# Kernel optimization log

Hardware: AMD Instinct MI355X
Metric: run time of the kernel (lower is better)

Reference implementation:

```python
import jax, jax.numpy as jnp
import numpy as np

D_MODEL = 1024
D_FF = 4096
EPS = 1e-5


def layer_norm(x, gamma, beta):
    mu = jnp.mean(x, axis=-1, keepdims=True)
    var = jnp.var(x, axis=-1, keepdims=True)
    return (x - mu) * jax.lax.rsqrt(var + EPS) * gamma + beta


def attention(x_q, x_kv, WQ, WK, WV, causal):
    Q = x_q @ WQ          # [B,Sq,D]
    K = x_kv @ WK         # [B,Sk,D]
    V = x_kv @ WV
    scale = 1.0 / jnp.sqrt(jnp.asarray(Q.shape[-1], Q.dtype))
    scores = jnp.einsum('bqd,bkd->bqk', Q, K) * scale
    if causal:
        Sq, Sk = scores.shape[-2], scores.shape[-1]
        mask = jnp.triu(jnp.full((Sq, Sk), -jnp.inf, scores.dtype), k=1)
        scores = scores + mask
    attn = jax.nn.softmax(scores, axis=-1)
    return jnp.einsum('bqk,bkd->bqd', attn, V)


def setup_inputs() -> dict:
    key = jax.random.key(0)
    ks = jax.random.split(key, 16)
    B, S = 4, 2048
    s = 0.02
    inp = {
        'y': jax.random.normal(ks[0], (B, S, D_MODEL), jnp.float32),
        'Z': jax.random.normal(ks[1], (B, S, D_MODEL), jnp.float32),
        'WQ1': jax.random.normal(ks[2], (D_MODEL, D_MODEL), jnp.float32) * s,
        'WK1': jax.random.normal(ks[3], (D_MODEL, D_MODEL), jnp.float32) * s,
        'WV1': jax.random.normal(ks[4], (D_MODEL, D_MODEL), jnp.float32) * s,
        'WQ2': jax.random.normal(ks[5], (D_MODEL, D_MODEL), jnp.float32) * s,
        'WK2': jax.random.normal(ks[6], (D_MODEL, D_MODEL), jnp.float32) * s,
        'WV2': jax.random.normal(ks[7], (D_MODEL, D_MODEL), jnp.float32) * s,
        'W_ff1': jax.random.normal(ks[8], (D_MODEL, D_FF), jnp.float32) * s,
        'b_ff1': jnp.zeros((D_FF,), jnp.float32),
        'W_ff2': jax.random.normal(ks[9], (D_FF, D_MODEL), jnp.float32) * s,
        'b_ff2': jnp.zeros((D_MODEL,), jnp.float32),
        'g1': jnp.ones((D_MODEL,), jnp.float32), 'be1': jnp.zeros((D_MODEL,), jnp.float32),
        'g2': jnp.ones((D_MODEL,), jnp.float32), 'be2': jnp.zeros((D_MODEL,), jnp.float32),
        'g3': jnp.ones((D_MODEL,), jnp.float32), 'be3': jnp.zeros((D_MODEL,), jnp.float32),
    }
    return inp


def reference(y, Z, WQ1, WK1, WV1, WQ2, WK2, WV2, W_ff1, b_ff1, W_ff2, b_ff2,
              g1, be1, g2, be2, g3, be3):
    # masked self-attention + add&norm
    y = layer_norm(y + attention(y, y, WQ1, WK1, WV1, causal=True), g1, be1)
    # cross-attention + add&norm
    y = layer_norm(y + attention(y, Z, WQ2, WK2, WV2, causal=False), g2, be2)
    # FFN + add&norm
    h = jax.nn.relu(y @ W_ff1 + b_ff1) @ W_ff2 + b_ff2
    y = layer_norm(y + h, g3, be3)
    return y
```

## Files before the change

kernel.cpp:

```cpp
#include <hip/hip_runtime.h>
#include <cstddef>

typedef unsigned short u16;
typedef __attribute__((ext_vector_type(8))) short bf16x8;
typedef __attribute__((ext_vector_type(4))) float f32x4;

__device__ __forceinline__ u16 f2bf(float f) {
  union { float f; unsigned u; } x; x.f = f;
  unsigned r = x.u + 0x7fffu + ((x.u >> 16) & 1u);
  return (u16)(r >> 16);
}
__device__ __forceinline__ float bf2f(u16 h) {
  union { unsigned u; float f; } x; x.u = ((unsigned)h) << 16;
  return x.f;
}

__device__ __forceinline__ void gll16(const u16* g, u16* ldsbase) {
  __builtin_amdgcn_global_load_lds(
      (const __attribute__((address_space(1))) void*)g,
      (__attribute__((address_space(3))) void*)ldsbase, 16, 0, 0);
}

__global__ __launch_bounds__(256) void f32_to_bf16(const float* __restrict__ in,
                                                   u16* __restrict__ out, size_t n) {
  size_t i = (size_t)blockIdx.x * 256 + threadIdx.x;
  if (i < n) out[i] = f2bf(in[i]);
}

__global__ __launch_bounds__(256) void transpose_f32_bf16(const float* __restrict__ in,
                                                          u16* __restrict__ out,
                                                          int R, int C) {
  __shared__ float tile[32][33];
  int c0 = blockIdx.x * 32, r0 = blockIdx.y * 32;
  int tx = threadIdx.x & 31, ty = threadIdx.x >> 5;
  #pragma unroll
  for (int i = ty; i < 32; i += 8)
    tile[i][tx] = in[(size_t)(r0 + i) * C + c0 + tx];
  __syncthreads();
  #pragma unroll
  for (int i = ty; i < 32; i += 8)
    out[(size_t)(c0 + i) * R + r0 + tx] = f2bf(tile[tx][i]);
}

enum { EPI_F32 = 0, EPI_BF16 = 1, EPI_BF16_SCALE = 2,
       EPI_BIAS_RELU_BF16 = 3, EPI_BIAS_F32 = 4 };
enum { MODE_FULL = 0, MODE_TRI = 1, MODE_CAUSAL_K = 2 };

template <int EPI, int MODE>
__global__ __launch_bounds__(512) void gemm256(
    const u16* __restrict__ A, const u16* __restrict__ Bt,
    void* __restrict__ C0, const float* __restrict__ bias,
    int K, int lda, int ldb, int ldc,
    long long sA, long long sB, long long sC)
{
  __shared__ __align__(16) u16 lA[2][256 * 64];
  __shared__ __align__(16) u16 lB[2][256 * 64];

  const unsigned gx = gridDim.x, gxy = gridDim.x * gridDim.y;
  unsigned id = blockIdx.x + gx * blockIdx.y + gxy * blockIdx.z;
  const unsigned nb = gxy * gridDim.z;
  unsigned p = id;
  if ((nb & 7u) == 0u) p = (id & 7u) * (nb >> 3) + (id >> 3);
  int z, mi, ni;
  if constexpr (MODE == MODE_TRI) {
    z = (int)(p / gxy);
    int r = (int)(p % gxy);
    int m = 0;
    while ((m + 1) * (m + 2) / 2 <= r) m++;
    mi = m; ni = r - m * (m + 1) / 2;
  } else {
    z = (int)(p / gxy);
    const unsigned rem = p % gxy;
    mi = (int)(rem / gx);
    ni = (int)(rem % gx);
  }
  const int m0 = mi * 256, n0 = ni * 256;

  A  += (long long)z * sA;
  Bt += (long long)z * sB;

  int NT = K >> 6;
  if constexpr (MODE == MODE_CAUSAL_K) NT = (m0 + 256) >> 6;

  const int t    = threadIdx.x;
  const int lane = t & 63;
  const int wave = t >> 6;
  const int wr   = wave >> 2;
  const int wc   = wave & 3;
  const int quad = lane >> 4;
  const int lrow = lane & 15;

  const int srow = lane >> 3;
  const int scol = ((lane & 7) ^ srow) * 8;
  const u16* gAp = A  + (size_t)(m0 + wave * 8 + srow) * lda + scol;
  const u16* gBp = Bt + (size_t)(n0 + wave * 8 + srow) * ldb + scol;
  const size_t a64 = (size_t)64 * lda, b64 = (size_t)64 * ldb;
  const int lw = wave * 512;

  const int pg0 = (quad ^ (lrow & 7)) * 8;
  const int pg1 = pg0 ^ 32;
  const int rA = (wr * 128 + lrow) * 64;
  const int rB = (wc * 64 + lrow) * 64;

  f32x4 acc[8][4];
  const f32x4 zero = {0.f, 0.f, 0.f, 0.f};
  #pragma unroll
  for (int i = 0; i < 8; i++)
    #pragma unroll
    for (int j = 0; j < 4; j++) acc[i][j] = zero;

  auto stage = [&](int b, int s, int kt) {
    const int k = kt * 64;
    if (s == 0) {
      gll16(gBp + k,            &lB[b][lw]);
      gll16(gBp + k + b64,      &lB[b][4096 + lw]);
    } else if (s == 1) {
      gll16(gBp + k + 2 * b64,  &lB[b][8192 + lw]);
      gll16(gBp + k + 3 * b64,  &lB[b][12288 + lw]);
    } else if (s == 2) {
      gll16(gAp + k,            &lA[b][lw]);
      gll16(gAp + k + a64,      &lA[b][4096 + lw]);
    } else {
      gll16(gAp + k + 2 * a64,  &lA[b][8192 + lw]);
      gll16(gAp + k + 3 * a64,  &lA[b][12288 + lw]);
    }
  };

  stage(0, 0, 0); stage(0, 1, 0); stage(0, 2, 0); stage(0, 3, 0);
  if (NT > 1) {
    stage(1, 0, 1); stage(1, 1, 1); stage(1, 2, 1);
    asm volatile("s_waitcnt vmcnt(6)" ::: "memory");
  } else {
    asm volatile("s_waitcnt vmcnt(0)" ::: "memory");
  }
  __builtin_amdgcn_s_barrier();

  bf16x8 af[4][2], bfr[4][2];

  for (int kt = 0; kt < NT; ++kt) {
    const int bsel = kt & 1;
    const u16* sa = &lA[bsel][0];
    const u16* sb = &lB[bsel][0];

    #pragma unroll
    for (int mf = 0; mf < 4; ++mf) {
      af[mf][0] = *(const bf16x8*)(sa + rA + mf * 1024 + pg0);
      af[mf][1] = *(const bf16x8*)(sa + rA + mf * 1024 + pg1);
    }
    if (wc < 2) {
      #pragma unroll
      for (int nf = 0; nf < 4; ++nf) {
        bfr[nf][0] = *(const bf16x8*)(sb + rB + nf * 1024 + pg0);
        bfr[nf][1] = *(const bf16x8*)(sb + rB + nf * 1024 + pg1);
      }
    } else {
      #pragma unroll
      for (int nf = 0; nf < 2; ++nf) {
        bfr[nf][0] = *(const bf16x8*)(sb + rB + nf * 1024 + pg0);
        bfr[nf][1] = *(const bf16x8*)(sb + rB + nf * 1024 + pg1);
      }
    }
    if (kt + 1 < NT) stage(bsel ^ 1, 3, kt + 1);
    __builtin_amdgcn_s_barrier();
    asm volatile("s_waitcnt lgkmcnt(0)" ::: "memory");
    __builtin_amdgcn_sched_barrier(0);
    __builtin_amdgcn_s_setprio(1);
    #pragma unroll
    for (int mf = 0; mf < 4; ++mf)
      #pragma unroll
      for (int nf = 0; nf < 2; ++nf) {
        acc[mf][nf] = __builtin_amdgcn_mfma_f32_16x16x32_bf16(bfr[nf][0], af[mf][0], acc[mf][nf], 0, 0, 0);
        acc[mf][nf] = __builtin_amdgcn_mfma_f32_16x16x32_bf16(bfr[nf][1], af[mf][1], acc[mf][nf], 0, 0, 0);
      }
    __builtin_amdgcn_s_setprio(0);
    __builtin_amdgcn_s_barrier();

    if (wc >= 2) {
      #pragma unroll
      for (int nf = 2; nf < 4; ++nf) {
        bfr[nf][0] = *(const bf16x8*)(sb + rB + nf * 1024 + pg0);
        bfr[nf][1] = *(const bf16x8*)(sb + rB + nf * 1024 + pg1);
      }
    }
    if (kt + 2 < NT) stage(bsel, 0, kt + 2);
    __builtin_amdgcn_s_barrier();
    asm volatile("s_waitcnt lgkmcnt(0)" ::: "memory");
    __builtin_amdgcn_sched_barrier(0);
    __builtin_amdgcn_s_setprio(1);
    #pragma unroll
    for (int mf = 0; mf < 4; ++mf)
      #pragma unroll
      for (int nf = 2; nf < 4; ++nf) {
        acc[mf][nf] = __builtin_amdgcn_mfma_f32_16x16x32_bf16(bfr[nf][0], af[mf][0], acc[mf][nf], 0, 0, 0);
        acc[mf][nf] = __builtin_amdgcn_mfma_f32_16x16x32_bf16(bfr[nf][1], af[mf][1], acc[mf][nf], 0, 0, 0);
      }
    __builtin_amdgcn_s_setprio(0);
    __builtin_amdgcn_s_barrier();

    #pragma unroll
    for (int mf = 0; mf < 4; ++mf) {
      af[mf][0] = *(const bf16x8*)(sa + rA + (mf + 4) * 1024 + pg0);
      af[mf][1] = *(const bf16x8*)(sa + rA + (mf + 4) * 1024 + pg1);
    }
    if (kt + 2 < NT) stage(bsel, 1, kt + 2);
    __builtin_amdgcn_s_barrier();
    asm volatile("s_waitcnt lgkmcnt(0)" ::: "memory");
    __builtin_amdgcn_sched_barrier(0);
    __builtin_amdgcn_s_setprio(1);
    #pragma unroll
    for (int mf = 0; mf < 4; ++mf)
      #pragma unroll
      for (int nf = 2; nf < 4; ++nf) {
        acc[mf + 4][nf] = __builtin_amdgcn_mfma_f32_16x16x32_bf16(bfr[nf][0], af[mf][0], acc[mf + 4][nf], 0, 0, 0);
        acc[mf + 4][nf] = __builtin_amdgcn_mfma_f32_16x16x32_bf16(bfr[nf][1], af[mf][1], acc[mf + 4][nf], 0, 0, 0);
      }
    __builtin_amdgcn_s_setprio(0);
    __builtin_amdgcn_s_barrier();

    if (kt + 2 < NT) {
      stage(bsel, 2, kt + 2);
      asm volatile("s_waitcnt vmcnt(6)" ::: "memory");
    } else if (kt + 1 < NT) {
      asm volatile("s_waitcnt vmcnt(0)" ::: "memory");
    }
    __builtin_amdgcn_s_barrier();
    __builtin_amdgcn_s_setprio(1);
    #pragma unroll
    for (int mf = 0; mf < 4; ++mf)
      #pragma unroll
      for (int nf = 0; nf < 2; ++nf) {
        acc[mf + 4][nf] = __builtin_amdgcn_mfma_f32_16x16x32_bf16(bfr[nf][0], af[mf][0], acc[mf + 4][nf], 0, 0, 0);
        acc[mf + 4][nf] = __builtin_amdgcn_mfma_f32_16x16x32_bf16(bfr[nf][1], af[mf][1], acc[mf + 4][nf], 0, 0, 0);
      }
    __builtin_amdgcn_s_setprio(0);
    __builtin_amdgcn_s_barrier();
  }

  const size_t zoff = (size_t)((long long)z * sC);
  #pragma unroll
  for (int mf = 0; mf < 8; ++mf) {
    #pragma unroll
    for (int nf = 0; nf < 4; ++nf) {
      const size_t m  = (size_t)(m0 + wr * 128 + mf * 16 + lrow);
      const size_t nc = (size_t)(n0 + wc * 64 + nf * 16 + quad * 4);
      const size_t idx = zoff + m * (size_t)ldc + nc;
      f32x4 v = acc[mf][nf];
      if constexpr (EPI == EPI_F32) {
        *(float4*)((float*)C0 + idx) = make_float4(v[0], v[1], v[2], v[3]);
      } else if constexpr (EPI == EPI_BF16) {
        ushort4 o; o.x = f2bf(v[0]); o.y = f2bf(v[1]); o.z = f2bf(v[2]); o.w = f2bf(v[3]);
        *(ushort4*)((u16*)C0 + idx) = o;
      } else if constexpr (EPI == EPI_BF16_SCALE) {
        ushort4 o;
        o.x = f2bf(v[0] * 0.03125f); o.y = f2bf(v[1] * 0.03125f);
        o.z = f2bf(v[2] * 0.03125f); o.w = f2bf(v[3] * 0.03125f);
        *(ushort4*)((u16*)C0 + idx) = o;
      } else if constexpr (EPI == EPI_BIAS_RELU_BF16) {
        const float4 bb = *(const float4*)(bias + nc);
        float y0 = v[0] + bb.x, y1 = v[1] + bb.y, y2 = v[2] + bb.z, y3 = v[3] + bb.w;
        ushort4 o;
        o.x = f2bf(y0 > 0.f ? y0 : 0.f); o.y = f2bf(y1 > 0.f ? y1 : 0.f);
        o.z = f2bf(y2 > 0.f ? y2 : 0.f); o.w = f2bf(y3 > 0.f ? y3 : 0.f);
        *(ushort4*)((u16*)C0 + idx) = o;
      } else {
        const float4 bb = *(const float4*)(bias + nc);
        *(float4*)((float*)C0 + idx) =
            make_float4(v[0] + bb.x, v[1] + bb.y, v[2] + bb.z, v[3] + bb.w);
      }
    }
  }
}

__global__ __launch_bounds__(256) void softmax_bf16(u16* __restrict__ SP, int causal) {
  __shared__ float red[8];
  const int row = blockIdx.x;
  const int q = row & 2047;
  u16* p = SP + (size_t)row * 2048;
  const int t = threadIdx.x;
  const int base = t * 8;
  const int limit = causal ? (q + 1) : 2048;

  uint4 raw = *(const uint4*)(p + base);
  unsigned w[4] = {raw.x, raw.y, raw.z, raw.w};
  float v[8];
  #pragma unroll
  for (int j = 0; j < 4; j++) {
    union { unsigned u; float f; } lo, hi;
    lo.u = w[j] << 16; hi.u = w[j] & 0xffff0000u;
    v[2 * j] = lo.f; v[2 * j + 1] = hi.f;
  }
  #pragma unroll
  for (int j = 0; j < 8; j++) if (base + j >= limit) v[j] = -3.4e38f;

  float mx = v[0];
  #pragma unroll
  for (int j = 1; j < 8; j++) mx = fmaxf(mx, v[j]);
  #pragma unroll
  for (int o = 32; o > 0; o >>= 1) mx = fmaxf(mx, __shfl_down(mx, o));
  if ((t & 63) == 0) red[t >> 6] = mx;
  __syncthreads();
  mx = fmaxf(fmaxf(red[0], red[1]), fmaxf(red[2], red[3]));

  float s = 0.f;
  #pragma unroll
  for (int j = 0; j < 8; j++) { float e = __expf(v[j] - mx); v[j] = e; s += e; }
  #pragma unroll
  for (int o = 32; o > 0; o >>= 1) s += __shfl_down(s, o);
  if ((t & 63) == 0) red[4 + (t >> 6)] = s;
  __syncthreads();
  const float inv = 1.f / (red[4] + red[5] + red[6] + red[7]);

  unsigned o4[4];
  #pragma unroll
  for (int j = 0; j < 4; j++)
    o4[j] = (unsigned)f2bf(v[2 * j] * inv) | ((unsigned)f2bf(v[2 * j + 1] * inv) << 16);
  *(uint4*)(p + base) = make_uint4(o4[0], o4[1], o4[2], o4[3]);
}

template <int ABF>
__global__ __launch_bounds__(256) void ln_residual(const void* __restrict__ a_,
                                                   const float* __restrict__ b,
                                                   const float* __restrict__ g,
                                                   const float* __restrict__ be,
                                                   float* __restrict__ outf,
                                                   u16* __restrict__ outb) {
  __shared__ float red[8];
  const size_t base = (size_t)blockIdx.x * 1024;
  const int t = threadIdx.x;
  const int i0 = t * 4;

  float va[4];
  if constexpr (ABF) {
    const ushort4 h = *(const ushort4*)((const u16*)a_ + base + i0);
    va[0] = bf2f(h.x); va[1] = bf2f(h.y); va[2] = bf2f(h.z); va[3] = bf2f(h.w);
  } else {
    const float4 f = *(const float4*)((const float*)a_ + base + i0);
    va[0] = f.x; va[1] = f.y; va[2] = f.z; va[3] = f.w;
  }
  const float4 vb = *(const float4*)(b + base + i0);
  float v[4] = {va[0] + vb.x, va[1] + vb.y, va[2] + vb.z, va[3] + vb.w};

  float s = v[0] + v[1] + v[2] + v[3];
  #pragma unroll
  for (int o = 32; o > 0; o >>= 1) s += __shfl_down(s, o);
  if ((t & 63) == 0) red[t >> 6] = s;
  __syncthreads();
  const float mean = (red[0] + red[1] + red[2] + red[3]) * (1.f / 1024.f);

  float qq = 0.f;
  #pragma unroll
  for (int i = 0; i < 4; i++) { float d = v[i] - mean; qq += d * d; }
  #pragma unroll
  for (int o = 32; o > 0; o >>= 1) qq += __shfl_down(qq, o);
  if ((t & 63) == 0) red[4 + (t >> 6)] = qq;
  __syncthreads();
  const float rstd = rsqrtf((red[4] + red[5] + red[6] + red[7]) * (1.f / 1024.f) + 1e-5f);

  const float4 gg = *(const float4*)(g + i0);
  const float4 bb = *(const float4*)(be + i0);
  float y0 = (v[0] - mean) * rstd * gg.x + bb.x;
  float y1 = (v[1] - mean) * rstd * gg.y + bb.y;
  float y2 = (v[2] - mean) * rstd * gg.z + bb.z;
  float y3 = (v[3] - mean) * rstd * gg.w + bb.w;
  if (outf) *(float4*)(outf + base + i0) = make_float4(y0, y1, y2, y3);
  if (outb) {
    ushort4 o4; o4.x = f2bf(y0); o4.y = f2bf(y1); o4.z = f2bf(y2); o4.w = f2bf(y3);
    *(ushort4*)(outb + base + i0) = o4;
  }
}

extern "C" void kernel_launch(void* const* d_in, const int* in_sizes, int n_in,
                              void* d_out, int out_size, void* d_ws, size_t ws_size,
                              hipStream_t stream)
{
  const float* y_in = (const float*)d_in[0];
  const float* Z_in = (const float*)d_in[1];
  const float* WQ1  = (const float*)d_in[2];
  const float* WK1  = (const float*)d_in[3];
  const float* WV1  = (const float*)d_in[4];
  const float* WQ2  = (const float*)d_in[5];
  const float* WK2  = (const float*)d_in[6];
  const float* WV2  = (const float*)d_in[7];
  const float* Wff1 = (const float*)d_in[8];
  const float* bff1 = (const float*)d_in[9];
  const float* Wff2 = (const float*)d_in[10];
  const float* bff2 = (const float*)d_in[11];
  const float* g1  = (const float*)d_in[12];
  const float* be1 = (const float*)d_in[13];
  const float* g2  = (const float*)d_in[14];
  const float* be2 = (const float*)d_in[15];
  const float* g3  = (const float*)d_in[16];
  const float* be3 = (const float*)d_in[17];
  (void)in_sizes; (void)n_in; (void)out_size;

  constexpr int Bn = 4, S = 2048, D = 1024, DF = 4096;
  constexpr long long BS = (long long)Bn * S;
  const long long SD = (long long)S * D;
  const long long SS = (long long)S * S;
  const long long SD2 = (long long)S * 2 * D;

  char* ws = (char*)d_ws;
  size_t off = 0;
  auto alloc = [&](size_t bytes) -> char* {
    char* p = ws + off;
    off += (bytes + 255) & ~(size_t)255;
    return p;
  };

  u16* wq1t  = (u16*)alloc((size_t)D * D * 2);
  u16* wk1t  = (u16*)alloc((size_t)D * D * 2);
  u16* wv1t  = (u16*)alloc((size_t)D * D * 2);
  u16* wq2t  = (u16*)alloc((size_t)D * D * 2);
  u16* wk2t  = (u16*)alloc((size_t)D * D * 2);
  u16* wv2t  = (u16*)alloc((size_t)D * D * 2);
  u16* wff1t = (u16*)alloc((size_t)D * DF * 2);
  u16* wff2t = (u16*)alloc((size_t)D * DF * 2);
  u16* ybf   = (u16*)alloc((size_t)BS * D * 2);
  u16* zbf   = (u16*)alloc((size_t)BS * D * 2);
  u16* QKb   = (u16*)alloc((size_t)BS * 2 * D * 2);
  u16* Vtb   = (u16*)alloc((size_t)D * BS * 2);
  u16* SPb   = (u16*)alloc((size_t)Bn * S * S * 2);
  float* attnF = (float*)alloc((size_t)BS * D * 4);
  u16*   y1b = ybf;
  u16*   y2b = zbf;
  u16*   Hb  = QKb;
  float* Fb  = attnF;

  if (off > ws_size) return;

  const dim3 blk(256);
  const dim3 blk512(512);

  f32_to_bf16<<<dim3((unsigned)((BS * D) / 256)), blk, 0, stream>>>(y_in, ybf, (size_t)BS * D);
  f32_to_bf16<<<dim3((unsigned)((BS * D) / 256)), blk, 0, stream>>>(Z_in, zbf, (size_t)BS * D);
  transpose_f32_bf16<<<dim3(D / 32, D / 32), blk, 0, stream>>>(WQ1, wq1t, D, D);
  transpose_f32_bf16<<<dim3(D / 32, D / 32), blk, 0, stream>>>(WK1, wk1t, D, D);
  transpose_f32_bf16<<<dim3(D / 32, D / 32), blk, 0, stream>>>(WV1, wv1t, D, D);
  transpose_f32_bf16<<<dim3(D / 32, D / 32), blk, 0, stream>>>(WQ2, wq2t, D, D);
  transpose_f32_bf16<<<dim3(D / 32, D / 32), blk, 0, stream>>>(WK2, wk2t, D, D);
  transpose_f32_bf16<<<dim3(D / 32, D / 32), blk, 0, stream>>>(WV2, wv2t, D, D);
  transpose_f32_bf16<<<dim3(DF / 32, D / 32), blk, 0, stream>>>(Wff1, wff1t, D, DF);
  transpose_f32_bf16<<<dim3(D / 32, DF / 32), blk, 0, stream>>>(Wff2, wff2t, DF, D);

  gemm256<EPI_BF16, MODE_FULL><<<dim3(2 * D / 256, BS / 256, 1), blk512, 0, stream>>>(
      ybf, wq1t, QKb, nullptr, D, D, D, 2 * D, 0, 0, 0);
  gemm256<EPI_BF16, MODE_FULL><<<dim3((unsigned)(BS / 256), D / 256, 1), blk512, 0, stream>>>(
      wv1t, ybf, Vtb, nullptr, D, D, D, (int)BS, 0, 0, 0);
  gemm256<EPI_BF16_SCALE, MODE_TRI><<<dim3(36, 1, Bn), blk512, 0, stream>>>(
      QKb, QKb + D, SPb, nullptr, D, 2 * D, 2 * D, S, SD2, SD2, SS);
  softmax_bf16<<<dim3((unsigned)(Bn * S)), blk, 0, stream>>>(SPb, 1);
  gemm256<EPI_F32, MODE_CAUSAL_K><<<dim3(D / 256, S / 256, Bn), blk512, 0, stream>>>(
      SPb, Vtb, attnF, nullptr, S, S, (int)BS, D, SS, S, SD);
  ln_residual<0><<<dim3((unsigned)BS), blk, 0, stream>>>(y_in, attnF, g1, be1, nullptr, y1b);

  gemm256<EPI_BF16, MODE_FULL><<<dim3(D / 256, BS / 256, 1), blk512, 0, stream>>>(
      y1b, wq2t, QKb, nullptr, D, D, D, 2 * D, 0, 0, 0);
  gemm256<EPI_BF16, MODE_FULL><<<dim3(D / 256, BS / 256, 1), blk512, 0, stream>>>(
      zbf, wk2t, QKb + D, nullptr, D, D, D, 2 * D, 0, 0, 0);
  gemm256<EPI_BF16, MODE_FULL><<<dim3((unsigned)(BS / 256), D / 256, 1), blk512, 0, stream>>>(
      wv2t, zbf, Vtb, nullptr, D, D, D, (int)BS, 0, 0, 0);
  gemm256<EPI_BF16_SCALE, MODE_FULL><<<dim3(S / 256, S / 256, Bn), blk512, 0, stream>>>(
      QKb, QKb + D, SPb, nullptr, D, 2 * D, 2 * D, S, SD2, SD2, SS);
  softmax_bf16<<<dim3((unsigned)(Bn * S)), blk, 0, stream>>>(SPb, 0);
  gemm256<EPI_F32, MODE_FULL><<<dim3(D / 256, S / 256, Bn), blk512, 0, stream>>>(
      SPb, Vtb, attnF, nullptr, S, S, (int)BS, D, SS, S, SD);
  ln_residual<1><<<dim3((unsigned)BS), blk, 0, stream>>>(y1b, attnF, g2, be2, nullptr, y2b);

  gemm256<EPI_BIAS_RELU_BF16, MODE_FULL><<<dim3(DF / 256, BS / 256, 1), blk512, 0, stream>>>(
      y2b, wff1t, Hb, bff1, D, D, D, DF, 0, 0, 0);
  gemm256<EPI_BIAS_F32, MODE_FULL><<<dim3(D / 256, BS / 256, 1), blk512, 0, stream>>>(
      Hb, wff2t, Fb, bff2, DF, DF, DF, D, 0, 0, 0);
  ln_residual<1><<<dim3((unsigned)BS), blk, 0, stream>>>(y2b, Fb, g3, be3, (float*)d_out, nullptr);
}
```

Measured before the change: 870.7 us.

## Template GEMM tile shape and use 256x128 tiles for low-occupancy GEMMs

```diff
diff --git a/kernel.cpp b/kernel.cpp
--- a/kernel.cpp
+++ b/kernel.cpp
@@ -46,15 +46,22 @@
        EPI_BIAS_RELU_BF16 = 3, EPI_BIAS_F32 = 4 };
 enum { MODE_FULL = 0, MODE_TRI = 1, MODE_CAUSAL_K = 2 };
 
-template <int EPI, int MODE>
+template <int EPI, int MODE, int BM, int BN>
 __global__ __launch_bounds__(512) void gemm256(
     const u16* __restrict__ A, const u16* __restrict__ Bt,
     void* __restrict__ C0, const float* __restrict__ bias,
     int K, int lda, int ldb, int ldc,
     long long sA, long long sB, long long sC)
 {
-  __shared__ __align__(16) u16 lA[2][256 * 64];
-  __shared__ __align__(16) u16 lB[2][256 * 64];
+  constexpr int WM  = BM / 128;
+  constexpr int WN  = 8 / WM;
+  constexpr int CPW = BN / WN;
+  constexpr int NF  = CPW / 16;
+  constexpr int nBr = BN / 64;
+  constexpr int nAr = BM / 64;
+
+  __shared__ __align__(16) u16 lA[2][BM * 64];
+  __shared__ __align__(16) u16 lB[2][BN * 64];
 
   const unsigned gx = gridDim.x, gxy = gridDim.x * gridDim.y;
   unsigned id = blockIdx.x + gx * blockIdx.y + gxy * blockIdx.z;
@@ -66,27 +73,32 @@
     z = (int)(p / gxy);
     int r = (int)(p % gxy);
     int m = 0;
-    while ((m + 1) * (m + 2) / 2 <= r) m++;
-    mi = m; ni = r - m * (m + 1) / 2;
+    if constexpr (BN == 256) {
+      while ((m + 1) * (m + 2) / 2 <= r) m++;
+      mi = m; ni = r - m * (m + 1) / 2;
+    } else {
+      while ((m + 1) * (m + 2) <= r) m++;
+      mi = m; ni = r - m * (m + 1);
+    }
   } else {
     z = (int)(p / gxy);
     const unsigned rem = p % gxy;
     mi = (int)(rem / gx);
     ni = (int)(rem % gx);
   }
-  const int m0 = mi * 256, n0 = ni * 256;
+  const int m0 = mi * BM, n0 = ni * BN;
 
   A  += (long long)z * sA;
   Bt += (long long)z * sB;
 
   int NT = K >> 6;
-  if constexpr (MODE == MODE_CAUSAL_K) NT = (m0 + 256) >> 6;
+  if constexpr (MODE == MODE_CAUSAL_K) NT = (m0 + BM) >> 6;
 
   const int t    = threadIdx.x;
   const int lane = t & 63;
   const int wave = t >> 6;
-  const int wr   = wave >> 2;
-  const int wc   = wave & 3;
+  const int wr   = (WM == 1) ? 0 : (wave >> 2);
+  const int wc   = (WM == 1) ? wave : (wave & 3);
   const int quad = lane >> 4;
   const int lrow = lane & 15;
 
@@ -100,149 +112,227 @@
   const int pg0 = (quad ^ (lrow & 7)) * 8;
   const int pg1 = pg0 ^ 32;
   const int rA = (wr * 128 + lrow) * 64;
-  const int rB = (wc * 64 + lrow) * 64;
-
-  f32x4 acc[8][4];
+  const int rB = (wc * CPW + lrow) * 64;
+
+  f32x4 acc[8][NF];
   const f32x4 zero = {0.f, 0.f, 0.f, 0.f};
   #pragma unroll
   for (int i = 0; i < 8; i++)
     #pragma unroll
-    for (int j = 0; j < 4; j++) acc[i][j] = zero;
-
-  auto stage = [&](int b, int s, int kt) {
-    const int k = kt * 64;
-    if (s == 0) {
-      gll16(gBp + k,            &lB[b][lw]);
-      gll16(gBp + k + b64,      &lB[b][4096 + lw]);
-    } else if (s == 1) {
-      gll16(gBp + k + 2 * b64,  &lB[b][8192 + lw]);
-      gll16(gBp + k + 3 * b64,  &lB[b][12288 + lw]);
-    } else if (s == 2) {
-      gll16(gAp + k,            &lA[b][lw]);
-      gll16(gAp + k + a64,      &lA[b][4096 + lw]);
+    for (int j = 0; j < NF; j++) acc[i][j] = zero;
+
+  bf16x8 af[4][2];
+  bf16x8 bfr[NF][2];
+
+  if constexpr (BM == 256 && BN == 256) {
+    auto stage = [&](int b, int s, int kt) {
+      const int k = kt * 64;
+      if (s == 0) {
+        gll16(gBp + k,            &lB[b][lw]);
+        gll16(gBp + k + b64,      &lB[b][4096 + lw]);
+      } else if (s == 1) {
+        gll16(gBp + k + 2 * b64,  &lB[b][8192 + lw]);
+        gll16(gBp + k + 3 * b64,  &lB[b][12288 + lw]);
+      } else if (s == 2) {
+        gll16(gAp + k,            &lA[b][lw]);
+        gll16(gAp + k + a64,      &lA[b][4096 + lw]);
+      } else {
+        gll16(gAp + k + 2 * a64,  &lA[b][8192 + lw]);
+        gll16(gAp + k + 3 * a64,  &lA[b][12288 + lw]);
+      }
+    };
+
+    stage(0, 0, 0); stage(0, 1, 0); stage(0, 2, 0); stage(0, 3, 0);
+    if (NT > 1) {
+      stage(1, 0, 1); stage(1, 1, 1); stage(1, 2, 1);
+      asm volatile("s_waitcnt vmcnt(6)" ::: "memory");
     } else {
-      gll16(gAp + k + 2 * a64,  &lA[b][8192 + lw]);
-      gll16(gAp + k + 3 * a64,  &lA[b][12288 + lw]);
-    }
-  };
-
-  stage(0, 0, 0); stage(0, 1, 0); stage(0, 2, 0); stage(0, 3, 0);
-  if (NT > 1) {
-    stage(1, 0, 1); stage(1, 1, 1); stage(1, 2, 1);
-    asm volatile("s_waitcnt vmcnt(6)" ::: "memory");
+      asm volatile("s_waitcnt vmcnt(0)" ::: "memory");
+    }
+    __builtin_amdgcn_s_barrier();
+
+    for (int kt = 0; kt < NT; ++kt) {
+      const int bsel = kt & 1;
+      const u16* sa = &lA[bsel][0];
+      const u16* sb = &lB[bsel][0];
+
+      #pragma unroll
+      for (int mf = 0; mf < 4; ++mf) {
+        af[mf][0] = *(const bf16x8*)(sa + rA + mf * 1024 + pg0);
+        af[mf][1] = *(const bf16x8*)(sa + rA + mf * 1024 + pg1);
+      }
+      if (wc < 2) {
+        #pragma unroll
+        for (int nf = 0; nf < 4; ++nf) {
+          bfr[nf][0] = *(const bf16x8*)(sb + rB + nf * 1024 + pg0);
+          bfr[nf][1] = *(const bf16x8*)(sb + rB + nf * 1024 + pg1);
+        }
+      } else {
+        #pragma unroll
+        for (int nf = 0; nf < 2; ++nf) {
+          bfr[nf][0] = *(const bf16x8*)(sb + rB + nf * 1024 + pg0);
+          bfr[nf][1] = *(const bf16x8*)(sb + rB + nf * 1024 + pg1);
+        }
+      }
+      if (kt + 1 < NT) stage(bsel ^ 1, 3, kt + 1);
+      __builtin_amdgcn_s_barrier();
+      asm volatile("s_waitcnt lgkmcnt(0)" ::: "memory");
+      __builtin_amdgcn_sched_barrier(0);
+      __builtin_amdgcn_s_setprio(1);
+      #pragma unroll
+      for (int mf = 0; mf < 4; ++mf)
+        #pragma unroll
+        for (int nf = 0; nf < 2; ++nf) {
+          acc[mf][nf] = __builtin_amdgcn_mfma_f32_16x16x32_bf16(bfr[nf][0], af[mf][0], acc[mf][nf], 0, 0, 0);
+          acc[mf][nf] = __builtin_amdgcn_mfma_f32_16x16x32_bf16(bfr[nf][1], af[mf][1], acc[mf][nf], 0, 0, 0);
+        }
+      __builtin_amdgcn_s_setprio(0);
+      __builtin_amdgcn_s_barrier();
+
+      if (wc >= 2) {
+        #pragma unroll
+        for (int nf = 2; nf < 4; ++nf) {
+          bfr[nf][0] = *(const bf16x8*)(sb + rB + nf * 1024 + pg0);
+          bfr[nf][1] = *(const bf16x8*)(sb + rB + nf * 1024 + pg1);
+        }
+      }
+      if (kt + 2 < NT) stage(bsel, 0, kt + 2);
+      __builtin_amdgcn_s_barrier();
+      asm volatile("s_waitcnt lgkmcnt(0)" ::: "memory");
+      __builtin_amdgcn_sched_barrier(0);
+      __builtin_amdgcn_s_setprio(1);
+      #pragma unroll
+      for (int mf = 0; mf < 4; ++mf)
+        #pragma unroll
+        for (int nf = 2; nf < 4; ++nf) {
+          acc[mf][nf] = __builtin_amdgcn_mfma_f32_16x16x32_bf16(bfr[nf][0], af[mf][0], acc[mf][nf], 0, 0, 0);
+          acc[mf][nf] = __builtin_amdgcn_mfma_f32_16x16x32_bf16(bfr[nf][1], af[mf][1], acc[mf][nf], 0, 0, 0);
+        }
+      __builtin_amdgcn_s_setprio(0);
+      __builtin_amdgcn_s_barrier();
+
+      #pragma unroll
+      for (int mf = 0; mf < 4; ++mf) {
+        af[mf][0] = *(const bf16x8*)(sa + rA + (mf + 4) * 1024 + pg0);
+        af[mf][1] = *(const bf16x8*)(sa + rA + (mf + 4) * 1024 + pg1);
+      }
+      if (kt + 2 < NT) stage(bsel, 1, kt + 2);
+      __builtin_amdgcn_s_barrier();
+      asm volatile("s_waitcnt lgkmcnt(0)" ::: "memory");
+      __builtin_amdgcn_sched_barrier(0);
+      __builtin_amdgcn_s_setprio(1);
+      #pragma unroll
+      for (int mf = 0; mf < 4; ++mf)
+        #pragma unroll
+        for (int nf = 2; nf < 4; ++nf) {
+          acc[mf + 4][nf] = __builtin_amdgcn_mfma_f32_16x16x32_bf16(bfr[nf][0], af[mf][0], acc[mf + 4][nf], 0, 0, 0);
+          acc[mf + 4][nf] = __builtin_amdgcn_mfma_f32_16x16x32_bf16(bfr[nf][1], af[mf][1], acc[mf + 4][nf], 0, 0, 0);
+        }
+      __builtin_amdgcn_s_setprio(0);
+      __builtin_amdgcn_s_barrier();
+
+      if (kt + 2 < NT) {
+        stage(bsel, 2, kt + 2);
+        asm volatile("s_waitcnt vmcnt(6)" ::: "memory");
+      } else if (kt + 1 < NT) {
+        asm volatile("s_waitcnt vmcnt(0)" ::: "memory");
+      }
+      __builtin_amdgcn_s_barrier();
+      __builtin_amdgcn_s_setprio(1);
+      #pragma unroll
+      for (int mf = 0; mf < 4; ++mf)
+        #pragma unroll
+        for (int nf = 0; nf < 2; ++nf) {
+          acc[mf + 4][nf] = __builtin_amdgcn_mfma_f32_16x16x32_bf16(bfr[nf][0], af[mf][0], acc[mf + 4][nf], 0, 0, 0);
+          acc[mf + 4][nf] = __builtin_amdgcn_mfma_f32_16x16x32_bf16(bfr[nf][1], af[mf][1], acc[mf + 4][nf], 0, 0, 0);
+        }
+      __builtin_amdgcn_s_setprio(0);
+      __builtin_amdgcn_s_barrier();
+    }
   } else {
-    asm volatile("s_waitcnt vmcnt(0)" ::: "memory");
-  }
-  __builtin_amdgcn_s_barrier();
-
-  bf16x8 af[4][2], bfr[4][2];
-
-  for (int kt = 0; kt < NT; ++kt) {
-    const int bsel = kt & 1;
-    const u16* sa = &lA[bsel][0];
-    const u16* sb = &lB[bsel][0];
-
-    #pragma unroll
-    for (int mf = 0; mf < 4; ++mf) {
-      af[mf][0] = *(const bf16x8*)(sa + rA + mf * 1024 + pg0);
-      af[mf][1] = *(const bf16x8*)(sa + rA + mf * 1024 + pg1);
-    }
-    if (wc < 2) {
-      #pragma unroll
-      for (int nf = 0; nf < 4; ++nf) {
-        bfr[nf][0] = *(const bf16x8*)(sb + rB + nf * 1024 + pg0);
-        bfr[nf][1] = *(const bf16x8*)(sb + rB + nf * 1024 + pg1);
-      }
+    auto stage3 = [&](int b, int h, int kt) {
+      const int k = kt * 64;
+      #pragma unroll
+      for (int s = 0; s < 3; ++s) {
+        const int rg = h * 3 + s;
+        if (rg < nBr) gll16(gBp + k + (size_t)rg * b64, &lB[b][rg * 4096 + lw]);
+        else          gll16(gAp + k + (size_t)(rg - nBr) * a64, &lA[b][(rg - nBr) * 4096 + lw]);
+      }
+    };
+
+    stage3(0, 0, 0); stage3(0, 1, 0);
+    if (NT > 1) {
+      stage3(1, 0, 1);
+      asm volatile("s_waitcnt vmcnt(3)" ::: "memory");
     } else {
+      asm volatile("s_waitcnt vmcnt(0)" ::: "memory");
+    }
+    __builtin_amdgcn_s_barrier();
+
+    for (int kt = 0; kt < NT; ++kt) {
+      const int bsel = kt & 1;
+      const u16* sa = &lA[bsel][0];
+      const u16* sb = &lB[bsel][0];
+
+      #pragma unroll
+      for (int mf = 0; mf < 4; ++mf) {
+        af[mf][0] = *(const bf16x8*)(sa + rA + mf * 1024 + pg0);
+        af[mf][1] = *(const bf16x8*)(sa + rA + mf * 1024 + pg1);
+      }
       #pragma unroll
       for (int nf = 0; nf < 2; ++nf) {
         bfr[nf][0] = *(const bf16x8*)(sb + rB + nf * 1024 + pg0);
         bfr[nf][1] = *(const bf16x8*)(sb + rB + nf * 1024 + pg1);
       }
-    }
-    if (kt + 1 < NT) stage(bsel ^ 1, 3, kt + 1);
-    __builtin_amdgcn_s_barrier();
-    asm volatile("s_waitcnt lgkmcnt(0)" ::: "memory");
-    __builtin_amdgcn_sched_barrier(0);
-    __builtin_amdgcn_s_setprio(1);
-    #pragma unroll
-    for (int mf = 0; mf < 4; ++mf)
-      #pragma unroll
-      for (int nf = 0; nf < 2; ++nf) {
-        acc[mf][nf] = __builtin_amdgcn_mfma_f32_16x16x32_bf16(bfr[nf][0], af[mf][0], acc[mf][nf], 0, 0, 0);
-        acc[mf][nf] = __builtin_amdgcn_mfma_f32_16x16x32_bf16(bfr[nf][1], af[mf][1], acc[mf][nf], 0, 0, 0);
-      }
-    __builtin_amdgcn_s_setprio(0);
-    __builtin_amdgcn_s_barrier();
-
-    if (wc >= 2) {
-      #pragma unroll
-      for (int nf = 2; nf < 4; ++nf) {
-        bfr[nf][0] = *(const bf16x8*)(sb + rB + nf * 1024 + pg0);
-        bfr[nf][1] = *(const bf16x8*)(sb + rB + nf * 1024 + pg1);
-      }
-    }
-    if (kt + 2 < NT) stage(bsel, 0, kt + 2);
-    __builtin_amdgcn_s_barrier();
-    asm volatile("s_waitcnt lgkmcnt(0)" ::: "memory");
-    __builtin_amdgcn_sched_barrier(0);
-    __builtin_amdgcn_s_setprio(1);
-    #pragma unroll
-    for (int mf = 0; mf < 4; ++mf)
-      #pragma unroll
-      for (int nf = 2; nf < 4; ++nf) {
-        acc[mf][nf] = __builtin_amdgcn_mfma_f32_16x16x32_bf16(bfr[nf][0], af[mf][0], acc[mf][nf], 0, 0, 0);
-        acc[mf][nf] = __builtin_amdgcn_mfma_f32_16x16x32_bf16(bfr[nf][1], af[mf][1], acc[mf][nf], 0, 0, 0);
-      }
-    __builtin_amdgcn_s_setprio(0);
-    __builtin_amdgcn_s_barrier();
-
-    #pragma unroll
-    for (int mf = 0; mf < 4; ++mf) {
-      af[mf][0] = *(const bf16x8*)(sa + rA + (mf + 4) * 1024 + pg0);
-      af[mf][1] = *(const bf16x8*)(sa + rA + (mf + 4) * 1024 + pg1);
-    }
-    if (kt + 2 < NT) stage(bsel, 1, kt + 2);
-    __builtin_amdgcn_s_barrier();
-    asm volatile("s_waitcnt lgkmcnt(0)" ::: "memory");
-    __builtin_amdgcn_sched_barrier(0);
-    __builtin_amdgcn_s_setprio(1);
-    #pragma unroll
-    for (int mf = 0; mf < 4; ++mf)
-      #pragma unroll
-      for (int nf = 2; nf < 4; ++nf) {
-        acc[mf + 4][nf] = __builtin_amdgcn_mfma_f32_16x16x32_bf16(bfr[nf][0], af[mf][0], acc[mf + 4][nf], 0, 0, 0);
-        acc[mf + 4][nf] = __builtin_amdgcn_mfma_f32_16x16x32_bf16(bfr[nf][1], af[mf][1], acc[mf + 4][nf], 0, 0, 0);
-      }
-    __builtin_amdgcn_s_setprio(0);
-    __builtin_amdgcn_s_barrier();
-
-    if (kt + 2 < NT) {
-      stage(bsel, 2, kt + 2);
-      asm volatile("s_waitcnt vmcnt(6)" ::: "memory");
-    } else if (kt + 1 < NT) {
-      asm volatile("s_waitcnt vmcnt(0)" ::: "memory");
-    }
-    __builtin_amdgcn_s_barrier();
-    __builtin_amdgcn_s_setprio(1);
-    #pragma unroll
-    for (int mf = 0; mf < 4; ++mf)
-      #pragma unroll
-      for (int nf = 0; nf < 2; ++nf) {
-        acc[mf + 4][nf] = __builtin_amdgcn_mfma_f32_16x16x32_bf16(bfr[nf][0], af[mf][0], acc[mf + 4][nf], 0, 0, 0);
-        acc[mf + 4][nf] = __builtin_amdgcn_mfma_f32_16x16x32_bf16(bfr[nf][1], af[mf][1], acc[mf + 4][nf], 0, 0, 0);
-      }
-    __builtin_amdgcn_s_setprio(0);
-    __builtin_amdgcn_s_barrier();
+      if (kt + 1 < NT) stage3(bsel ^ 1, 1, kt + 1);
+      __builtin_amdgcn_s_barrier();
+      asm volatile("s_waitcnt lgkmcnt(0)" ::: "memory");
+      __builtin_amdgcn_sched_barrier(0);
+      __builtin_amdgcn_s_setprio(1);
+      #pragma unroll
+      for (int mf = 0; mf < 4; ++mf)
+        #pragma unroll
+        for (int nf = 0; nf < 2; ++nf) {
+          acc[mf][nf] = __builtin_amdgcn_mfma_f32_16x16x32_bf16(bfr[nf][0], af[mf][0], acc[mf][nf], 0, 0, 0);
+          acc[mf][nf] = __builtin_amdgcn_mfma_f32_16x16x32_bf16(bfr[nf][1], af[mf][1], acc[mf][nf], 0, 0, 0);
+        }
+      __builtin_amdgcn_s_setprio(0);
+      __builtin_amdgcn_s_barrier();
+
+      #pragma unroll
+      for (int mf = 0; mf < 4; ++mf) {
+        af[mf][0] = *(const bf16x8*)(sa + rA + (mf + 4) * 1024 + pg0);
+        af[mf][1] = *(const bf16x8*)(sa + rA + (mf + 4) * 1024 + pg1);
+      }
+      if (kt + 2 < NT) {
+        stage3(bsel, 0, kt + 2);
+        asm volatile("s_waitcnt vmcnt(3)" ::: "memory");
+      } else if (kt + 1 < NT) {
+        asm volatile("s_waitcnt vmcnt(0)" ::: "memory");
+      }
+      __builtin_amdgcn_s_barrier();
+      asm volatile("s_waitcnt lgkmcnt(0)" ::: "memory");
+      __builtin_amdgcn_sched_barrier(0);
+      __builtin_amdgcn_s_setprio(1);
+      #pragma unroll
+      for (int mf = 0; mf < 4; ++mf)
+        #pragma unroll
+        for (int nf = 0; nf < 2; ++nf) {
+          acc[mf + 4][nf] = __builtin_amdgcn_mfma_f32_16x16x32_bf16(bfr[nf][0], af[mf][0], acc[mf + 4][nf], 0, 0, 0);
+          acc[mf + 4][nf] = __builtin_amdgcn_mfma_f32_16x16x32_bf16(bfr[nf][1], af[mf][1], acc[mf + 4][nf], 0, 0, 0);
+        }
+      __builtin_amdgcn_s_setprio(0);
+      __builtin_amdgcn_s_barrier();
+    }
   }
 
   const size_t zoff = (size_t)((long long)z * sC);
   #pragma unroll
   for (int mf = 0; mf < 8; ++mf) {
     #pragma unroll
-    for (int nf = 0; nf < 4; ++nf) {
+    for (int nf = 0; nf < NF; ++nf) {
       const size_t m  = (size_t)(m0 + wr * 128 + mf * 16 + lrow);
-      const size_t nc = (size_t)(n0 + wc * 64 + nf * 16 + quad * 4);
+      const size_t nc = (size_t)(n0 + wc * CPW + nf * 16 + quad * 4);
       const size_t idx = zoff + m * (size_t)ldc + nc;
       f32x4 v = acc[mf][nf];
       if constexpr (EPI == EPI_F32) {
@@ -278,19 +368,25 @@
   u16* p = SP + (size_t)row * 2048;
   const int t = threadIdx.x;
   const int base = t * 8;
-  const int limit = causal ? (q + 1) : 2048;
-
-  uint4 raw = *(const uint4*)(p + base);
-  unsigned w[4] = {raw.x, raw.y, raw.z, raw.w};
+  const int limit  = causal ? (q + 1) : 2048;
+  const int wlimit = causal ? (((q >> 8) + 1) << 8) : 2048;
+
   float v[8];
-  #pragma unroll
-  for (int j = 0; j < 4; j++) {
-    union { unsigned u; float f; } lo, hi;
-    lo.u = w[j] << 16; hi.u = w[j] & 0xffff0000u;
-    v[2 * j] = lo.f; v[2 * j + 1] = hi.f;
-  }
-  #pragma unroll
-  for (int j = 0; j < 8; j++) if (base + j >= limit) v[j] = -3.4e38f;
+  if (base < limit) {
+    uint4 raw = *(const uint4*)(p + base);
+    unsigned w[4] = {raw.x, raw.y, raw.z, raw.w};
+    #pragma unroll
+    for (int j = 0; j < 4; j++) {
+      union { unsigned u; float f; } lo, hi;
+      lo.u = w[j] << 16; hi.u = w[j] & 0xffff0000u;
+      v[2 * j] = lo.f; v[2 * j + 1] = hi.f;
+    }
+    #pragma unroll
+    for (int j = 0; j < 8; j++) if (base + j >= limit) v[j] = -3.4e38f;
+  } else {
+    #pragma unroll
+    for (int j = 0; j < 8; j++) v[j] = -3.4e38f;
+  }
 
   float mx = v[0];
   #pragma unroll
@@ -310,11 +406,13 @@
   __syncthreads();
   const float inv = 1.f / (red[4] + red[5] + red[6] + red[7]);
 
-  unsigned o4[4];
-  #pragma unroll
-  for (int j = 0; j < 4; j++)
-    o4[j] = (unsigned)f2bf(v[2 * j] * inv) | ((unsigned)f2bf(v[2 * j + 1] * inv) << 16);
-  *(uint4*)(p + base) = make_uint4(o4[0], o4[1], o4[2], o4[3]);
+  if (base < wlimit) {
+    unsigned o4[4];
+    #pragma unroll
+    for (int j = 0; j < 4; j++)
+      o4[j] = (unsigned)f2bf(v[2 * j] * inv) | ((unsigned)f2bf(v[2 * j + 1] * inv) << 16);
+    *(uint4*)(p + base) = make_uint4(o4[0], o4[1], o4[2], o4[3]);
+  }
 }
 
 template <int ABF>
@@ -442,33 +540,33 @@
   transpose_f32_bf16<<<dim3(DF / 32, D / 32), blk, 0, stream>>>(Wff1, wff1t, D, DF);
   transpose_f32_bf16<<<dim3(D / 32, DF / 32), blk, 0, stream>>>(Wff2, wff2t, DF, D);
 
-  gemm256<EPI_BF16, MODE_FULL><<<dim3(2 * D / 256, BS / 256, 1), blk512, 0, stream>>>(
+  gemm256<EPI_BF16, MODE_FULL, 256, 256><<<dim3(2 * D / 256, BS / 256, 1), blk512, 0, stream>>>(
       ybf, wq1t, QKb, nullptr, D, D, D, 2 * D, 0, 0, 0);
-  gemm256<EPI_BF16, MODE_FULL><<<dim3((unsigned)(BS / 256), D / 256, 1), blk512, 0, stream>>>(
+  gemm256<EPI_BF16, MODE_FULL, 128, 256><<<dim3((unsigned)(BS / 256), D / 128, 1), blk512, 0, stream>>>(
       wv1t, ybf, Vtb, nullptr, D, D, D, (int)BS, 0, 0, 0);
-  gemm256<EPI_BF16_SCALE, MODE_TRI><<<dim3(36, 1, Bn), blk512, 0, stream>>>(
+  gemm256<EPI_BF16_SCALE, MODE_TRI, 256, 128><<<dim3(72, 1, Bn), blk512, 0, stream>>>(
       QKb, QKb + D, SPb, nullptr, D, 2 * D, 2 * D, S, SD2, SD2, SS);
   softmax_bf16<<<dim3((unsigned)(Bn * S)), blk, 0, stream>>>(SPb, 1);
-  gemm256<EPI_F32, MODE_CAUSAL_K><<<dim3(D / 256, S / 256, Bn), blk512, 0, stream>>>(
+  gemm256<EPI_F32, MODE_CAUSAL_K, 256, 128><<<dim3(D / 128, S / 256, Bn), blk512, 0, stream>>>(
       SPb, Vtb, attnF, nullptr, S, S, (int)BS, D, SS, S, SD);
   ln_residual<0><<<dim3((unsigned)BS), blk, 0, stream>>>(y_in, attnF, g1, be1, nullptr, y1b);
 
-  gemm256<EPI_BF16, MODE_FULL><<<dim3(D / 256, BS / 256, 1), blk512, 0, stream>>>(
+  gemm256<EPI_BF16, MODE_FULL, 256, 128><<<dim3(D / 128, BS / 256, 1), blk512, 0, stream>>>(
       y1b, wq2t, QKb, nullptr, D, D, D, 2 * D, 0, 0, 0);
-  gemm256<EPI_BF16, MODE_FULL><<<dim3(D / 256, BS / 256, 1), blk512, 0, stream>>>(
+  gemm256<EPI_BF16, MODE_FULL, 256, 128><<<dim3(D / 128, BS / 256, 1), blk512, 0, stream>>>(
       zbf, wk2t, QKb + D, nullptr, D, D, D, 2 * D, 0, 0, 0);
-  gemm256<EPI_BF16, MODE_FULL><<<dim3((unsigned)(BS / 256), D / 256, 1), blk512, 0, stream>>>(
+  gemm256<EPI_BF16, MODE_FULL, 128, 256><<<dim3((unsigned)(BS / 256), D / 128, 1), blk512, 0, stream>>>(
       wv2t, zbf, Vtb, nullptr, D, D, D, (int)BS, 0, 0, 0);
-  gemm256<EPI_BF16_SCALE, MODE_FULL><<<dim3(S / 256, S / 256, Bn), blk512, 0, stream>>>(
+  gemm256<EPI_BF16_SCALE, MODE_FULL, 256, 256><<<dim3(S / 256, S / 256, Bn), blk512, 0, stream>>>(
       QKb, QKb + D, SPb, nullptr, D, 2 * D, 2 * D, S, SD2, SD2, SS);
   softmax_bf16<<<dim3((unsigned)(Bn * S)), blk, 0, stream>>>(SPb, 0);
-  gemm256<EPI_F32, MODE_FULL><<<dim3(D / 256, S / 256, Bn), blk512, 0, stream>>>(
+  gemm256<EPI_F32, MODE_FULL, 256, 128><<<dim3(D / 128, S / 256, Bn), blk512, 0, stream>>>(
       SPb, Vtb, attnF, nullptr, S, S, (int)BS, D, SS, S, SD);
   ln_residual<1><<<dim3((unsigned)BS), blk, 0, stream>>>(y1b, attnF, g2, be2, nullptr, y2b);
 
-  gemm256<EPI_BIAS_RELU_BF16, MODE_FULL><<<dim3(DF / 256, BS / 256, 1), blk512, 0, stream>>>(
+  gemm256<EPI_BIAS_RELU_BF16, MODE_FULL, 256, 256><<<dim3(DF / 256, BS / 256, 1), blk512, 0, stream>>>(
       y2b, wff1t, Hb, bff1, D, D, D, DF, 0, 0, 0);
-  gemm256<EPI_BIAS_F32, MODE_FULL><<<dim3(D / 256, BS / 256, 1), blk512, 0, stream>>>(
+  gemm256<EPI_BIAS_F32, MODE_FULL, 256, 128><<<dim3(D / 128, BS / 256, 1), blk512, 0, stream>>>(
       Hb, wff2t, Fb, bff2, DF, DF, DF, D, 0, 0, 0);
   ln_residual<1><<<dim3((unsigned)BS), blk, 0, stream>>>(y2b, Fb, g3, be3, (float*)d_out, nullptr);
 }
```

Measured after the change: 740.6 us. -14.9%, faster.
